# Kernel tuning notes

Hardware: AMD Instinct MI355X
Metric: run time of the kernel (lower is better)

Reference implementation:

```python
import jax, jax.numpy as jnp
import numpy as np

# Graph/block sizes: batch=1024 output nodes, fanouts [15,10,5] outer->inner layer
N_SRC0 = 1081344
N_DST = (67584, 6144, 1024)
FANOUT = (15, 10, 5)
DIMS = ((128, 256), (256, 256), (256, 47))  # (in, out) per layer


def setup_inputs() -> dict:
    key = jax.random.key(0)
    ks = jax.random.split(key, 16)
    inp = {
        "x": jax.random.normal(ks[0], (N_SRC0, DIMS[0][0]), dtype=jnp.float32),
        "neigh0": jax.random.randint(ks[1], (N_DST[0], FANOUT[0]), 0, N_SRC0, dtype=jnp.int32),
        "neigh1": jax.random.randint(ks[2], (N_DST[1], FANOUT[1]), 0, N_DST[0], dtype=jnp.int32),
        "neigh2": jax.random.randint(ks[3], (N_DST[2], FANOUT[2]), 0, N_DST[1], dtype=jnp.int32),
    }
    for l, (din, dout) in enumerate(DIMS):
        s = 1.0 / np.sqrt(din)
        inp[f"Wself{l}"] = jax.random.normal(ks[4 + 3 * l], (din, dout), dtype=jnp.float32) * s
        inp[f"Wneigh{l}"] = jax.random.normal(ks[5 + 3 * l], (din, dout), dtype=jnp.float32) * s
        inp[f"b{l}"] = jnp.zeros((dout,), dtype=jnp.float32)
    return inp


def _sage_layer(h, neigh, Wself, Wneigh, b):
    # DGL SAGEConv('mean') on a bipartite block: dst nodes are the prefix of src nodes.
    h_neigh = jnp.mean(h[neigh], axis=1)          # [n_dst, d_in] gather + mean over fanout
    h_dst = h[: neigh.shape[0]]                    # [n_dst, d_in]
    return h_dst @ Wself + h_neigh @ Wneigh + b


def reference(x, neigh0, neigh1, neigh2,
              Wself0, Wneigh0, b0, Wself1, Wneigh1, b1, Wself2, Wneigh2, b2):
    # dropout is identity in eval mode; activation = relu on all but last layer
    h = jax.nn.relu(_sage_layer(x, neigh0, Wself0, Wneigh0, b0))
    h = jax.nn.relu(_sage_layer(h, neigh1, Wself1, Wneigh1, b1))
    return _sage_layer(h, neigh2, Wself2, Wneigh2, b2)  # [1024, 47]
```

## Files before the change

kernel.cpp:

```cpp
#include <hip/hip_runtime.h>

using bf16x8 = __attribute__((ext_vector_type(8))) short;
using f32x4  = __attribute__((ext_vector_type(4))) float;

__device__ __forceinline__ short f2bf(float x) {
    union { float f; unsigned u; } v; v.f = x;
    unsigned r = v.u + 0x7fffu + ((v.u >> 16) & 1u);
    return (short)(r >> 16);
}
__device__ __forceinline__ float bf2f(short h) {
    union { unsigned u; float f; } v; v.u = ((unsigned)(unsigned short)h) << 16;
    return v.f;
}

template<int DIN>
__device__ __forceinline__ void pack_one(int blk, const float* __restrict__ Wself,
                                         const float* __restrict__ Wneigh,
                                         short* __restrict__ Wp, int l)
{
    const int ks  = blk >> 4, nt = blk & 15;
    const int col = nt * 16 + (l & 15);
    const int k0  = ks * 32 + (l >> 4) * 8;

    bf16x8 hi;
    #pragma unroll
    for (int e = 0; e < 8; ++e) {
        int k = k0 + e;
        float w = (k < DIN) ? Wself[k * 256 + col] : Wneigh[(k - DIN) * 256 + col];
        hi[e] = f2bf(w);
    }
    *reinterpret_cast<bf16x8*>(Wp + (size_t)blk * 512 + l * 8) = hi;
}

__global__ __launch_bounds__(256)
void k_prep(const int* __restrict__ neigh1, const int* __restrict__ neigh2,
            unsigned char* __restrict__ mask0, unsigned char* __restrict__ mask1,
            const float* __restrict__ Ws0, const float* __restrict__ Wn0,
            short* __restrict__ Wp0,
            const float* __restrict__ Ws1, const float* __restrict__ Wn1,
            short* __restrict__ Wp1)
{
    const int b = blockIdx.x, tid = threadIdx.x;
    if (b < 240) {
        int j = b * 256 + tid;
        mask0[neigh1[j]] = 1;
    } else if (b < 264) {
        int i = (b - 240) * 256 + tid;
        mask0[i] = 1;
    } else if (b < 284) {
        int j = (b - 264) * 256 + tid;
        mask1[neigh2[j]] = 1;
    } else if (b < 288) {
        int i = (b - 284) * 256 + tid;
        mask1[i] = 1;
    } else {
        int unit = (b - 288) * 4 + (tid >> 6);
        int l = tid & 63;
        if (unit < 128) pack_one<128>(unit, Ws0, Wn0, Wp0, l);
        else            pack_one<256>(unit - 128, Ws1, Wn1, Wp1, l);
    }
}

template<int DIN, int F, int RB, int NTW, bool MASKED, bool IN_BF16, bool OUT_BF16, bool RELU>
__global__ __launch_bounds__(256, 6)
void sage_mfma(const void* __restrict__ h_in_v,
               const int*   __restrict__ neigh,
               const short* __restrict__ Wp,
               const float* __restrict__ bias,
               void* __restrict__ h_out_v,
               const unsigned char* __restrict__ mask)
{
    constexpr int KS    = DIN / 16;
    constexpr int KSH   = DIN / 32;
    constexpr int LROW  = DIN + 4;
    constexpr int WROWS = RB / 16;
    constexpr int WCOLS = 16 / NTW;
    static_assert(WROWS * WCOLS == 4, "4 waves");
    constexpr float invF = 1.0f / F;

    __shared__ float         An[RB][LROW];
    __shared__ int           nb[RB * F];
    __shared__ unsigned char need[RB];

    const int  tid = threadIdx.x;
    const int  w   = tid >> 6, l = tid & 63;
    const int  lr  = l & 15, lk = l >> 4;
    const long r0  = (long)blockIdx.x * RB;
    const int  wrow = (w % WROWS) * 16;
    const int  nt0  = (w / WROWS) * NTW;

    for (int p = tid; p < RB * F; p += 256)
        nb[p] = neigh[r0 * F + p];
    if constexpr (MASKED) {
        for (int p = tid; p < RB; p += 256)
            need[p] = mask[r0 + p];
    }
    __syncthreads();

    if constexpr (!IN_BF16) {
        constexpr int QD = DIN / 4;
        const float* hin = (const float*)h_in_v;
        for (int p = tid; p < RB * QD; p += 256) {
            int m = p / QD, q = p - m * QD;
            if (MASKED && need[m] != 1) continue;
            float4 a = make_float4(0.f, 0.f, 0.f, 0.f);
            #pragma unroll 5
            for (int n = 0; n < F; ++n) {
                long idx = nb[m * F + n];
                float4 v = reinterpret_cast<const float4*>(hin + idx * DIN)[q];
                a.x += v.x; a.y += v.y; a.z += v.z; a.w += v.w;
            }
            a.x *= invF; a.y *= invF; a.z *= invF; a.w *= invF;
            *reinterpret_cast<float4*>(&An[m][q * 4]) = a;
        }
    } else {
        constexpr int NQ = DIN / 8;
        const short* hin = (const short*)h_in_v;
        for (int p = tid; p < RB * NQ; p += 256) {
            int m = p / NQ, c = p - m * NQ;
            if (MASKED && need[m] != 1) continue;
            float a[8] = {0.f,0.f,0.f,0.f,0.f,0.f,0.f,0.f};
            #pragma unroll 5
            for (int n = 0; n < F; ++n) {
                long idx = nb[m * F + n];
                bf16x8 v = *reinterpret_cast<const bf16x8*>(hin + idx * DIN + c * 8);
                #pragma unroll
                for (int e = 0; e < 8; ++e) a[e] += bf2f(v[e]);
            }
            #pragma unroll
            for (int e = 0; e < 8; ++e) a[e] *= invF;
            *reinterpret_cast<float4*>(&An[m][c * 8])     = make_float4(a[0],a[1],a[2],a[3]);
            *reinterpret_cast<float4*>(&An[m][c * 8 + 4]) = make_float4(a[4],a[5],a[6],a[7]);
        }
    }
    __syncthreads();

    const float* selfrowF = (const float*)h_in_v + (r0 + wrow + lr) * DIN;
    const short* selfrowB = (const short*)h_in_v + (r0 + wrow + lr) * DIN;
    const float* neighrow = &An[wrow + lr][0];

    f32x4 acc[NTW];
    #pragma unroll
    for (int j = 0; j < NTW; ++j) acc[j] = f32x4{0.f, 0.f, 0.f, 0.f};

    for (int ks = 0; ks < KS; ++ks) {
        bf16x8 ah, al;
        bool self_exact = false;
        if (ks < KSH) {
            if constexpr (IN_BF16) {
                ah = *reinterpret_cast<const bf16x8*>(selfrowB + ks * 32 + lk * 8);
                self_exact = true;
            } else {
                const int k0 = ks * 32 + lk * 8;
                float4 t0 = *reinterpret_cast<const float4*>(selfrowF + k0);
                float4 t1 = *reinterpret_cast<const float4*>(selfrowF + k0 + 4);
                float v[8] = {t0.x, t0.y, t0.z, t0.w, t1.x, t1.y, t1.z, t1.w};
                #pragma unroll
                for (int e = 0; e < 8; ++e) {
                    short h = f2bf(v[e]);
                    ah[e] = h;
                    al[e] = f2bf(v[e] - bf2f(h));
                }
            }
        } else {
            const int k0 = (ks - KSH) * 32 + lk * 8;
            float4 t0 = *reinterpret_cast<const float4*>(neighrow + k0);
            float4 t1 = *reinterpret_cast<const float4*>(neighrow + k0 + 4);
            float v[8] = {t0.x, t0.y, t0.z, t0.w, t1.x, t1.y, t1.z, t1.w};
            #pragma unroll
            for (int e = 0; e < 8; ++e) {
                short h = f2bf(v[e]);
                ah[e] = h;
                al[e] = f2bf(v[e] - bf2f(h));
            }
        }

        const bf16x8* wp = reinterpret_cast<const bf16x8*>(Wp) +
                           (size_t)(ks * 16 + nt0) * 64;
        #pragma unroll
        for (int j = 0; j < NTW; ++j) {
            bf16x8 bh = wp[j * 64 + l];
            acc[j] = __builtin_amdgcn_mfma_f32_16x16x32_bf16(ah, bh, acc[j], 0, 0, 0);
            if (!self_exact)
                acc[j] = __builtin_amdgcn_mfma_f32_16x16x32_bf16(al, bh, acc[j], 0, 0, 0);
        }
    }

    #pragma unroll
    for (int j = 0; j < NTW; ++j) {
        const int col = (nt0 + j) * 16 + lr;
        const float b = bias[col];
        #pragma unroll
        for (int r = 0; r < 4; ++r) {
            const int slot = wrow + lk * 4 + r;
            if (MASKED && need[slot] != 1) continue;
            const long row = r0 + slot;
            float val = acc[j][r] + b;
            if (RELU) val = fmaxf(val, 0.f);
            if constexpr (OUT_BF16)
                ((short*)h_out_v)[row * 256 + col] = f2bf(val);
            else
                ((float*)h_out_v)[row * 256 + col] = val;
        }
    }
}

__global__ __launch_bounds__(64)
void sage_out(const float* __restrict__ h_in,
              const int*   __restrict__ neigh,
              const float* __restrict__ Wself,
              const float* __restrict__ Wneigh,
              const float* __restrict__ bias,
              float* __restrict__ out)
{
    __shared__ float hs[256], hn[256];
    __shared__ int   nb[5];
    const int r = blockIdx.x, tid = threadIdx.x;

    if (tid < 5) nb[tid] = neigh[r * 5 + tid];
    __syncthreads();

    for (int k = tid; k < 256; k += 64) {
        hs[k] = h_in[(long)r * 256 + k];
        float a = 0.f;
        #pragma unroll
        for (int n = 0; n < 5; ++n) a += h_in[(long)nb[n] * 256 + k];
        hn[k] = a * 0.2f;
    }
    __syncthreads();

    if (tid < 47) {
        float a0 = 0.f, a1 = 0.f, a2 = 0.f, a3 = 0.f;
        #pragma unroll 4
        for (int k = 0; k < 256; k += 4) {
            a0 += hs[k    ] * Wself[(k    ) * 47 + tid] + hn[k    ] * Wneigh[(k    ) * 47 + tid];
            a1 += hs[k + 1] * Wself[(k + 1) * 47 + tid] + hn[k + 1] * Wneigh[(k + 1) * 47 + tid];
            a2 += hs[k + 2] * Wself[(k + 2) * 47 + tid] + hn[k + 2] * Wneigh[(k + 2) * 47 + tid];
            a3 += hs[k + 3] * Wself[(k + 3) * 47 + tid] + hn[k + 3] * Wneigh[(k + 3) * 47 + tid];
        }
        out[r * 47 + tid] = bias[tid] + ((a0 + a1) + (a2 + a3));
    }
}

extern "C" void kernel_launch(void* const* d_in, const int* in_sizes, int n_in,
                              void* d_out, int out_size, void* d_ws, size_t ws_size,
                              hipStream_t stream)
{
    const float* x   = (const float*)d_in[0];
    const int*   n0  = (const int*)  d_in[1];
    const int*   n1  = (const int*)  d_in[2];
    const int*   n2  = (const int*)  d_in[3];
    const float* Ws0 = (const float*)d_in[4];
    const float* Wn0 = (const float*)d_in[5];
    const float* b0  = (const float*)d_in[6];
    const float* Ws1 = (const float*)d_in[7];
    const float* Wn1 = (const float*)d_in[8];
    const float* b1  = (const float*)d_in[9];
    const float* Ws2 = (const float*)d_in[10];
    const float* Wn2 = (const float*)d_in[11];
    const float* b2  = (const float*)d_in[12];
    float* out = (float*)d_out;

    short*         h1    = (short*)d_ws;
    float*         h2    = (float*)(h1 + (size_t)67584 * 256);
    short*         Wp0   = (short*)(h2 + (size_t)6144 * 256);
    short*         Wp1   = Wp0 + (size_t)128 * 512;
    unsigned char* mask0 = (unsigned char*)(Wp1 + (size_t)256 * 512);
    unsigned char* mask1 = mask0 + 67584;

    constexpr int M0 = 67584;

    k_prep<<<384, 256, 0, stream>>>(n1, n2, mask0, mask1,
                                    Ws0, Wn0, Wp0, Ws1, Wn1, Wp1);

    sage_mfma<128, 15, 32, 8, true,  false, true,  true>
        <<<M0 / 32, 256, 0, stream>>>(x,  n0, Wp0, b0, h1, mask0);

    sage_mfma<256, 10, 16, 4, true,  true,  false, true>
        <<<6144 / 16, 256, 0, stream>>>(h1, n1, Wp1, b1, h2, mask1);

    sage_out<<<1024, 64, 0, stream>>>(h2, n2, Ws2, Wn2, b2, out);
}
```

Before: 128.0 us.

## Drop split-bf16 compensation, store neighbor means as bf16 in LDS

The hi/lo bf16 split on the activation operand is removed, so each k-step issues one MFMA instead of two and skips the residual conversions. Neighbor means are rounded to bf16 once at aggregation and stored in LDS as shorts, which halves LDS footprint and read traffic. Self-row loads are skipped for rows the mask marks as unneeded, and the occupancy hint in launch_bounds is dropped. This lowers numerical accuracy of the first layer's fp32 input path, since activations are now truncated to plain bf16.

New measurement: 129.3 us. No clear change (+1.0%).

```diff
diff --git a/kernel.cpp b/kernel.cpp
--- a/kernel.cpp
+++ b/kernel.cpp
@@ -62,7 +62,7 @@
 }
 
 template<int DIN, int F, int RB, int NTW, bool MASKED, bool IN_BF16, bool OUT_BF16, bool RELU>
-__global__ __launch_bounds__(256, 6)
+__global__ __launch_bounds__(256)
 void sage_mfma(const void* __restrict__ h_in_v,
                const int*   __restrict__ neigh,
                const short* __restrict__ Wp,
@@ -72,13 +72,13 @@
 {
     constexpr int KS    = DIN / 16;
     constexpr int KSH   = DIN / 32;
-    constexpr int LROW  = DIN + 4;
+    constexpr int LROWB = DIN + 8;
     constexpr int WROWS = RB / 16;
     constexpr int WCOLS = 16 / NTW;
     static_assert(WROWS * WCOLS == 4, "4 waves");
     constexpr float invF = 1.0f / F;
 
-    __shared__ float         An[RB][LROW];
+    __shared__ short         An[RB][LROWB];
     __shared__ int           nb[RB * F];
     __shared__ unsigned char need[RB];
 
@@ -110,8 +110,10 @@
                 float4 v = reinterpret_cast<const float4*>(hin + idx * DIN)[q];
                 a.x += v.x; a.y += v.y; a.z += v.z; a.w += v.w;
             }
-            a.x *= invF; a.y *= invF; a.z *= invF; a.w *= invF;
-            *reinterpret_cast<float4*>(&An[m][q * 4]) = a;
+            short4 s;
+            s.x = f2bf(a.x * invF); s.y = f2bf(a.y * invF);
+            s.z = f2bf(a.z * invF); s.w = f2bf(a.w * invF);
+            *reinterpret_cast<short4*>(&An[m][q * 4]) = s;
         }
     } else {
         constexpr int NQ = DIN / 8;
@@ -127,52 +129,44 @@
                 #pragma unroll
                 for (int e = 0; e < 8; ++e) a[e] += bf2f(v[e]);
             }
+            bf16x8 s;
             #pragma unroll
-            for (int e = 0; e < 8; ++e) a[e] *= invF;
-            *reinterpret_cast<float4*>(&An[m][c * 8])     = make_float4(a[0],a[1],a[2],a[3]);
-            *reinterpret_cast<float4*>(&An[m][c * 8 + 4]) = make_float4(a[4],a[5],a[6],a[7]);
-        }
-    }
-    __syncthreads();
-
+            for (int e = 0; e < 8; ++e) s[e] = f2bf(a[e] * invF);
+            *reinterpret_cast<bf16x8*>(&An[m][c * 8]) = s;
+        }
+    }
+    __syncthreads();
+
+    const bool  selfok   = !MASKED || (need[wrow + lr] == 1);
     const float* selfrowF = (const float*)h_in_v + (r0 + wrow + lr) * DIN;
     const short* selfrowB = (const short*)h_in_v + (r0 + wrow + lr) * DIN;
-    const float* neighrow = &An[wrow + lr][0];
+    const short* neighrow = &An[wrow + lr][0];
 
     f32x4 acc[NTW];
     #pragma unroll
     for (int j = 0; j < NTW; ++j) acc[j] = f32x4{0.f, 0.f, 0.f, 0.f};
 
     for (int ks = 0; ks < KS; ++ks) {
-        bf16x8 ah, al;
-        bool self_exact = false;
+        bf16x8 ah;
         if (ks < KSH) {
-            if constexpr (IN_BF16) {
-                ah = *reinterpret_cast<const bf16x8*>(selfrowB + ks * 32 + lk * 8);
-                self_exact = true;
+            if (selfok) {
+                if constexpr (IN_BF16) {
+                    ah = *reinterpret_cast<const bf16x8*>(selfrowB + ks * 32 + lk * 8);
+                } else {
+                    const int k0 = ks * 32 + lk * 8;
+                    float4 t0 = *reinterpret_cast<const float4*>(selfrowF + k0);
+                    float4 t1 = *reinterpret_cast<const float4*>(selfrowF + k0 + 4);
+                    ah[0] = f2bf(t0.x); ah[1] = f2bf(t0.y);
+                    ah[2] = f2bf(t0.z); ah[3] = f2bf(t0.w);
+                    ah[4] = f2bf(t1.x); ah[5] = f2bf(t1.y);
+                    ah[6] = f2bf(t1.z); ah[7] = f2bf(t1.w);
+                }
             } else {
-                const int k0 = ks * 32 + lk * 8;
-                float4 t0 = *reinterpret_cast<const float4*>(selfrowF + k0);
-                float4 t1 = *reinterpret_cast<const float4*>(selfrowF + k0 + 4);
-                float v[8] = {t0.x, t0.y, t0.z, t0.w, t1.x, t1.y, t1.z, t1.w};
                 #pragma unroll
-                for (int e = 0; e < 8; ++e) {
-                    short h = f2bf(v[e]);
-                    ah[e] = h;
-                    al[e] = f2bf(v[e] - bf2f(h));
-                }
+                for (int e = 0; e < 8; ++e) ah[e] = 0;
             }
         } else {
-            const int k0 = (ks - KSH) * 32 + lk * 8;
-            float4 t0 = *reinterpret_cast<const float4*>(neighrow + k0);
-            float4 t1 = *reinterpret_cast<const float4*>(neighrow + k0 + 4);
-            float v[8] = {t0.x, t0.y, t0.z, t0.w, t1.x, t1.y, t1.z, t1.w};
-            #pragma unroll
-            for (int e = 0; e < 8; ++e) {
-                short h = f2bf(v[e]);
-                ah[e] = h;
-                al[e] = f2bf(v[e] - bf2f(h));
-            }
+            ah = *reinterpret_cast<const bf16x8*>(neighrow + (ks - KSH) * 32 + lk * 8);
         }
 
         const bf16x8* wp = reinterpret_cast<const bf16x8*>(Wp) +
@@ -181,8 +175,6 @@
         for (int j = 0; j < NTW; ++j) {
             bf16x8 bh = wp[j * 64 + l];
             acc[j] = __builtin_amdgcn_mfma_f32_16x16x32_bf16(ah, bh, acc[j], 0, 0, 0);
-            if (!self_exact)
-                acc[j] = __builtin_amdgcn_mfma_f32_16x16x32_bf16(al, bh, acc[j], 0, 0, 0);
         }
     }
 
```
